# Kernel optimization log

Measured on AMD Instinct MI355X. Metric: run time of the kernel, lower is better.

The kernel has to match this reference:

```python
import jax, jax.numpy as jnp
import numpy as np

B, S, D, E, TOPK = 4, 2048, 1024, 8, 2


def setup_inputs() -> dict:
    key = jax.random.key(0)
    k1, k2, k3 = jax.random.split(key, 3)
    scale = 1.0 / np.sqrt(D)
    return {
        "x": jax.random.normal(k1, (B, S, D), dtype=jnp.float32),
        "gate_w": jax.random.normal(k2, (D, E), dtype=jnp.float32) * scale,
        "gate_b": jnp.zeros((E,), dtype=jnp.float32),
        "expert_w": jax.random.normal(k3, (E, D, D), dtype=jnp.float32) * scale,
        "expert_b": jnp.zeros((E, D), dtype=jnp.float32),
        "top_k": TOPK,
    }


def reference(x, gate_w, gate_b, expert_w, expert_b, top_k):
    # Gating: softmax over experts, then top-k expert indices per token.
    logits = x @ gate_w + gate_b                      # [B, S, E]
    probs = jax.nn.softmax(logits, axis=-1)
    _, top_idx = jax.lax.top_k(probs, top_k)          # [B, S, top_k]
    # Binary membership mask (original multiplies by mask, NOT gate probs).
    mask = jax.nn.one_hot(top_idx, probs.shape[-1], dtype=x.dtype).sum(axis=-2)  # [B, S, E]
    # Dense per-expert linear on all tokens (as in the original loop).
    expert_out = jnp.einsum('bsd,edf->bsef', x, expert_w) + expert_b  # [B, S, E, D]
    # Mask-multiply-accumulate over experts.
    return jnp.einsum('bse,bsef->bsf', mask, expert_out)             # [B, S, D]
```

## Files before the change

### kernel.cpp

```cpp
#include <hip/hip_runtime.h>
#include <stdint.h>

#define T_TOK 8192
#define DD    1024
#define EN    8
#define CPAD  16

#define BM 128
#define BN 128
#define BK 64
#define NT (DD / BK)
#define NWG 4096

#define GATE_NB 512

#define AS1 __attribute__((address_space(1)))
#define AS3 __attribute__((address_space(3)))

typedef __bf16 v8bf __attribute__((ext_vector_type(8)));
typedef float  v4f  __attribute__((ext_vector_type(4)));

__device__ __forceinline__ uint16_t f2b(float f) {
  uint32_t u = __builtin_bit_cast(uint32_t, f);
  u += 0x7FFFu + ((u >> 16) & 1u);
  return (uint16_t)(u >> 16);
}
__device__ __forceinline__ float b2f(uint16_t h) {
  uint32_t u = (uint32_t)h << 16;
  return __builtin_bit_cast(float, u);
}

template <bool WRITE_PIDX>
__global__ __launch_bounds__(256) void prep_kernel(
    const float* __restrict__ x, const float* __restrict__ gw,
    const float* __restrict__ gb, uint16_t* __restrict__ xb,
    int* __restrict__ counts, int* __restrict__ lists, int* __restrict__ pidx,
    const float* __restrict__ w, uint16_t* __restrict__ wt) {
  extern __shared__ __align__(16) uint8_t smem[];
  const int bid = blockIdx.x;
  const int tid = threadIdx.x;

  if (bid >= GATE_NB) {
    float (*tile)[65] = (float(*)[65])smem;
    const int tb = bid - GATE_NB;
    const int e = tb >> 8;
    const int rem = tb & 255;
    const int f0 = (rem & 15) * 64, d0 = (rem >> 4) * 64;
    const float* wsrc = w + ((size_t)e << 20);
    uint16_t* wdst = wt + ((size_t)e << 20);
    const int r4 = tid >> 4;
    const int c4 = (tid & 15) * 4;
#pragma unroll
    for (int i = 0; i < 4; ++i) {
      int row = i * 16 + r4;
      const float4 v = *(const float4*)(wsrc + (size_t)(d0 + row) * DD + f0 + c4);
      tile[row][c4 + 0] = v.x; tile[row][c4 + 1] = v.y;
      tile[row][c4 + 2] = v.z; tile[row][c4 + 3] = v.w;
    }
    __syncthreads();
#pragma unroll
    for (int i = 0; i < 4; ++i) {
      int f = i * 16 + r4;
      ushort4 h;
      h.x = f2b(tile[c4 + 0][f]); h.y = f2b(tile[c4 + 1][f]);
      h.z = f2b(tile[c4 + 2][f]); h.w = f2b(tile[c4 + 3][f]);
      *(ushort4*)(wdst + (size_t)(f0 + f) * DD + d0 + c4) = h;
    }
    return;
  }

  float* sgwt = (float*)smem;
  float (*sx)[DD] = (float(*)[DD])(smem + 32768);
  int* se1 = (int*)(smem + 49152);
  int* se2 = (int*)(smem + 49152 + 64);

#pragma unroll
  for (int i = 0; i < 8; ++i) {
    const int j4 = i * 256 + tid;
    const float4 v = ((const float4*)gw)[j4];
    const int d = j4 >> 1;
    const int e0 = (j4 & 1) * 4;
    sgwt[(e0 + 0) * DD + d] = v.x;
    sgwt[(e0 + 1) * DD + d] = v.y;
    sgwt[(e0 + 2) * DD + d] = v.z;
    sgwt[(e0 + 3) * DD + d] = v.w;
  }
  __syncthreads();

  const int t0 = bid * 16;
  const int wid = tid >> 6, lane = tid & 63;

  for (int r = 0; r < 4; ++r) {
    const int tt = t0 + wid * 4 + r;
    const float4* xg = (const float4*)(x + (size_t)tt * DD);
    float4* sxv = (float4*)sx[wid];
    ushort4* xbv = (ushort4*)(xb + (size_t)tt * DD);
#pragma unroll
    for (int i = 0; i < 4; ++i) {
      float4 v = xg[i * 64 + lane];
      sxv[i * 64 + lane] = v;
      ushort4 h;
      h.x = f2b(v.x); h.y = f2b(v.y); h.z = f2b(v.z); h.w = f2b(v.w);
      xbv[i * 64 + lane] = h;
    }
    asm volatile("s_waitcnt lgkmcnt(0)" ::: "memory");

    double part[8];
#pragma unroll
    for (int e = 0; e < 8; ++e) part[e] = 0.0;
#pragma unroll
    for (int c = 0; c < 16; ++c) {
      const double xd = (double)sx[wid][c * 64 + lane];
#pragma unroll
      for (int e = 0; e < 8; ++e)
        part[e] += xd * (double)sgwt[e * DD + c * 64 + lane];
    }
#pragma unroll
    for (int off = 1; off < 64; off <<= 1) {
#pragma unroll
      for (int e = 0; e < 8; ++e) part[e] += __shfl_xor(part[e], off);
    }
    if (lane == 0) {
      double lg[8];
#pragma unroll
      for (int i = 0; i < 8; ++i) lg[i] = part[i] + (double)gb[i];
      int e1 = 0; double m1 = lg[0];
#pragma unroll
      for (int i = 1; i < 8; ++i) if (lg[i] > m1) { m1 = lg[i]; e1 = i; }
      int e2 = 0; double m2 = -1.0e300;
#pragma unroll
      for (int i = 0; i < 8; ++i) if (i != e1 && lg[i] > m2) { m2 = lg[i]; e2 = i; }
      se1[wid * 4 + r] = e1;
      se2[wid * 4 + r] = e2;
    }
  }
  __syncthreads();

  if (tid < EN) {
    int cnt = 0;
#pragma unroll
    for (int i = 0; i < 16; ++i) cnt += (se1[i] == tid) + (se2[i] == tid);
    int base = atomicAdd(&counts[tid * CPAD], cnt);
    int* dst = lists + tid * T_TOK;
    for (int i = 0; i < 16; ++i) {
      if (se1[i] == tid) {
        if (WRITE_PIDX) pidx[2 * (t0 + i)] = tid * T_TOK + base;
        dst[base++] = t0 + i;
      }
      if (se2[i] == tid) {
        if (WRITE_PIDX) pidx[2 * (t0 + i) + 1] = tid * T_TOK + base;
        dst[base++] = t0 + i;
      }
    }
  }
}

template <bool ATOMIC>
__global__ __launch_bounds__(256, 4) void expert_gemm_kernel(
    const uint16_t* __restrict__ xb, const uint16_t* __restrict__ wt,
    const float* __restrict__ eb, const int* __restrict__ counts,
    const int* __restrict__ lists, uint16_t* __restrict__ dst,
    float* __restrict__ dstf) {
  const int orig = blockIdx.x;
  const int e = orig & 7;
  const int rem = orig >> 3;
  const int m0 = (rem >> 3) * BM;
  const int n0 = (rem & 7) * BN;
  const int cnt = counts[e * CPAD];
  if (m0 >= cnt) return;
  int rows = cnt - m0; if (rows > BM) rows = BM;
  int offsE = 0;
  if (!ATOMIC) {
#pragma unroll
    for (int i = 0; i < EN; ++i) offsE += (i < e) ? counts[i * CPAD] : 0;
  }

  __shared__ uint16_t sA[BM * BK];
  __shared__ uint16_t sB[BN * BK];
  __shared__ int toks[BM];

  const int tid = threadIdx.x;
  if (tid < BM) {
    int rr = tid < rows ? tid : 0;
    toks[tid] = lists[e * T_TOK + m0 + rr];
  }
  __syncthreads();

  const int lane = tid & 63;
  const int wid = tid >> 6;
  const int wm = wid >> 1;
  const int wn = wid & 1;

  v4f acc[4][4];
#pragma unroll
  for (int i = 0; i < 4; ++i)
#pragma unroll
    for (int j = 0; j < 4; ++j) acc[i][j] = (v4f){0.f, 0.f, 0.f, 0.f};

  const int koff = (((tid & 7) ^ ((tid >> 3) & 7)) << 3);
  const uint16_t* wte = wt + ((size_t)e << 20) + (size_t)n0 * DD;
  const uint16_t* aptr[4];
  const uint16_t* bptr[4];
#pragma unroll
  for (int i = 0; i < 4; ++i) {
    int row = i * 32 + (tid >> 3);
    aptr[i] = xb + (size_t)toks[row] * DD + koff;
    bptr[i] = wte + (size_t)row * DD + koff;
  }

  const int c0 = lane >> 4;
  const int rsel = lane & 15;
  const int rx = lane & 7;

  for (int kt = 0; kt < NT; ++kt) {
    const int k0 = kt * BK;
#pragma unroll
    for (int i = 0; i < 4; ++i) {
      int idx = i * 256 + tid;
      __builtin_amdgcn_global_load_lds(
          (const AS1 uint32_t*)(aptr[i] + k0),
          (AS3 uint32_t*)(sA + idx * 8), 16, 0, 0);
      __builtin_amdgcn_global_load_lds(
          (const AS1 uint32_t*)(bptr[i] + k0),
          (AS3 uint32_t*)(sB + idx * 8), 16, 0, 0);
    }
    __syncthreads();

#pragma unroll
    for (int kk = 0; kk < 2; ++kk) {
      v8bf af[4], bfr[4];
#pragma unroll
      for (int m = 0; m < 4; ++m) {
        int row_a = wm * 64 + m * 16 + rsel;
        af[m] = *(const v8bf*)(sA + row_a * BK + (((kk * 4 + c0) ^ rx) << 3));
      }
#pragma unroll
      for (int n = 0; n < 4; ++n) {
        int row_b = wn * 64 + n * 16 + rsel;
        bfr[n] = *(const v8bf*)(sB + row_b * BK + (((kk * 4 + c0) ^ rx) << 3));
      }
#pragma unroll
      for (int m = 0; m < 4; ++m)
#pragma unroll
        for (int n = 0; n < 4; ++n)
          acc[m][n] = __builtin_amdgcn_mfma_f32_16x16x32_bf16(
              af[m], bfr[n], acc[m][n], 0, 0, 0);
    }
    __syncthreads();
  }

  const int col = lane & 15, rq = lane >> 4;
  if (!ATOMIC) {
    uint16_t* base = dst + (size_t)(offsE + m0) * DD + n0 + wn * 64 + col;
#pragma unroll
    for (int m = 0; m < 4; ++m) {
#pragma unroll
      for (int j = 0; j < 4; ++j) {
        int trow = wm * 64 + m * 16 + rq * 4 + j;
        if (trow < rows) {
          uint16_t* orow = base + (size_t)trow * DD;
#pragma unroll
          for (int n = 0; n < 4; ++n) orow[n * 16] = f2b(acc[m][n][j]);
        }
      }
    }
  } else {
    float biasv[4];
#pragma unroll
    for (int n = 0; n < 4; ++n)
      biasv[n] = eb[e * DD + n0 + wn * 64 + n * 16 + col];
#pragma unroll
    for (int m = 0; m < 4; ++m) {
#pragma unroll
      for (int j = 0; j < 4; ++j) {
        int trow = wm * 64 + m * 16 + rq * 4 + j;
        if (trow < rows) {
          float* orow = dstf + (size_t)toks[trow] * DD + n0;
#pragma unroll
          for (int n = 0; n < 4; ++n)
            atomicAdd(orow + wn * 64 + n * 16 + col, acc[m][n][j] + biasv[n]);
        }
      }
    }
  }
}

__global__ __launch_bounds__(256) void combine_kernel(
    const uint16_t* __restrict__ wsO, const int* __restrict__ pidx,
    const int* __restrict__ counts, const float* __restrict__ eb,
    float* __restrict__ out) {
  __shared__ int soff[EN];
  const int tid = threadIdx.x;
  if (tid == 0) {
    int o = 0;
#pragma unroll
    for (int i = 0; i < EN; ++i) { soff[i] = o; o += counts[i * CPAD]; }
  }
  __syncthreads();
  const int t0 = blockIdx.x * 4;
#pragma unroll
  for (int r = 0; r < 4; ++r) {
    const int t = t0 + r;
    const int pi1 = pidx[2 * t], pi2 = pidx[2 * t + 1];
    const int e1 = pi1 >> 13, p1 = pi1 & (T_TOK - 1);
    const int e2 = pi2 >> 13, p2 = pi2 & (T_TOK - 1);
    ushort4 r1 = ((const ushort4*)(wsO + (size_t)(soff[e1] + p1) * DD))[tid];
    ushort4 r2 = ((const ushort4*)(wsO + (size_t)(soff[e2] + p2) * DD))[tid];
    v4f b1 = ((const v4f*)(eb + e1 * DD))[tid];
    v4f b2 = ((const v4f*)(eb + e2 * DD))[tid];
    v4f o;
    o[0] = b2f(r1.x) + b2f(r2.x) + b1[0] + b2[0];
    o[1] = b2f(r1.y) + b2f(r2.y) + b1[1] + b2[1];
    o[2] = b2f(r1.z) + b2f(r2.z) + b1[2] + b2[2];
    o[3] = b2f(r1.w) + b2f(r2.w) + b1[3] + b2[3];
    ((v4f*)(out + (size_t)t * DD))[tid] = o;
  }
}

extern "C" void kernel_launch(void* const* d_in, const int* in_sizes, int n_in,
                              void* d_out, int out_size, void* d_ws, size_t ws_size,
                              hipStream_t stream) {
  const float* x  = (const float*)d_in[0];
  const float* gw = (const float*)d_in[1];
  const float* gb = (const float*)d_in[2];
  const float* ew = (const float*)d_in[3];
  const float* ebias = (const float*)d_in[4];
  float* out = (float*)d_out;

  uint8_t* ws = (uint8_t*)d_ws;
  int* counts = (int*)ws;
  int* lists  = (int*)(ws + 512);
  int* pidx   = (int*)(ws + 512 + 262144);
  uint16_t* xb = (uint16_t*)(ws + 512 + 262144 + 65536);
  uint16_t* wt = (uint16_t*)(ws + 512 + 262144 + 65536 + 16777216);
  uint16_t* wsO = (uint16_t*)(ws + 512 + 262144 + 65536 + 2 * 16777216);
  const size_t need = 512ull + 262144 + 65536 + 2 * 16777216 +
                      (size_t)2 * T_TOK * DD * sizeof(uint16_t);
  const bool use_ws = ws_size >= need;

  hipMemsetAsync(counts, 0, 512, stream);
  if (use_ws) {
    prep_kernel<true><<<GATE_NB + 2048, 256, 49408, stream>>>(
        x, gw, gb, xb, counts, lists, pidx, ew, wt);
    expert_gemm_kernel<false><<<NWG, 256, 0, stream>>>(
        xb, wt, ebias, counts, lists, wsO, nullptr);
    combine_kernel<<<T_TOK / 4, 256, 0, stream>>>(wsO, pidx, counts, ebias, out);
  } else {
    hipMemsetAsync(d_out, 0, (size_t)out_size * sizeof(float), stream);
    prep_kernel<false><<<GATE_NB + 2048, 256, 49408, stream>>>(
        x, gw, gb, xb, counts, lists, pidx, ew, wt);
    expert_gemm_kernel<true><<<NWG, 256, 0, stream>>>(
        xb, wt, ebias, counts, lists, nullptr, out);
  }
}
```

Before: 92.93 us.

## Double-buffer LDS tiles in expert GEMM to overlap global loads with MFMA

```diff
diff --git a/kernel.cpp b/kernel.cpp
--- a/kernel.cpp
+++ b/kernel.cpp
@@ -156,7 +156,7 @@
 }
 
 template <bool ATOMIC>
-__global__ __launch_bounds__(256, 4) void expert_gemm_kernel(
+__global__ __launch_bounds__(256, 2) void expert_gemm_kernel(
     const uint16_t* __restrict__ xb, const uint16_t* __restrict__ wt,
     const float* __restrict__ eb, const int* __restrict__ counts,
     const int* __restrict__ lists, uint16_t* __restrict__ dst,
@@ -175,8 +175,8 @@
     for (int i = 0; i < EN; ++i) offsE += (i < e) ? counts[i * CPAD] : 0;
   }
 
-  __shared__ uint16_t sA[BM * BK];
-  __shared__ uint16_t sB[BN * BK];
+  __shared__ uint16_t sA[2 * BM * BK];
+  __shared__ uint16_t sB[2 * BN * BK];
   __shared__ int toks[BM];
 
   const int tid = threadIdx.x;
@@ -208,36 +208,53 @@
     bptr[i] = wte + (size_t)row * DD + koff;
   }
 
+#define STAGE(buf, k0)                                                          \
+  {                                                                             \
+    _Pragma("unroll")                                                           \
+    for (int i = 0; i < 4; ++i) {                                               \
+      int idx = i * 256 + tid;                                                  \
+      __builtin_amdgcn_global_load_lds(                                         \
+          (const AS1 uint32_t*)(aptr[i] + (k0)),                                \
+          (AS3 uint32_t*)(sA + (buf) * (BM * BK) + idx * 8), 16, 0, 0);         \
+      __builtin_amdgcn_global_load_lds(                                         \
+          (const AS1 uint32_t*)(bptr[i] + (k0)),                                \
+          (AS3 uint32_t*)(sB + (buf) * (BN * BK) + idx * 8), 16, 0, 0);         \
+    }                                                                           \
+  }
+
   const int c0 = lane >> 4;
   const int rsel = lane & 15;
   const int rx = lane & 7;
 
+  STAGE(0, 0);
+  int cur = 0;
   for (int kt = 0; kt < NT; ++kt) {
-    const int k0 = kt * BK;
-#pragma unroll
-    for (int i = 0; i < 4; ++i) {
-      int idx = i * 256 + tid;
-      __builtin_amdgcn_global_load_lds(
-          (const AS1 uint32_t*)(aptr[i] + k0),
-          (AS3 uint32_t*)(sA + idx * 8), 16, 0, 0);
-      __builtin_amdgcn_global_load_lds(
-          (const AS1 uint32_t*)(bptr[i] + k0),
-          (AS3 uint32_t*)(sB + idx * 8), 16, 0, 0);
-    }
-    __syncthreads();
-
+    if (kt + 1 < NT) {
+      STAGE(cur ^ 1, (kt + 1) * BK);
+      __builtin_amdgcn_sched_barrier(0);
+      asm volatile("s_waitcnt vmcnt(8)" ::: "memory");
+    } else {
+      __builtin_amdgcn_sched_barrier(0);
+      asm volatile("s_waitcnt vmcnt(0)" ::: "memory");
+    }
+    __builtin_amdgcn_sched_barrier(0);
+    __builtin_amdgcn_s_barrier();
+    __builtin_amdgcn_sched_barrier(0);
+
+    const uint16_t* a_base = sA + cur * (BM * BK);
+    const uint16_t* b_base = sB + cur * (BN * BK);
 #pragma unroll
     for (int kk = 0; kk < 2; ++kk) {
       v8bf af[4], bfr[4];
 #pragma unroll
       for (int m = 0; m < 4; ++m) {
         int row_a = wm * 64 + m * 16 + rsel;
-        af[m] = *(const v8bf*)(sA + row_a * BK + (((kk * 4 + c0) ^ rx) << 3));
+        af[m] = *(const v8bf*)(a_base + row_a * BK + (((kk * 4 + c0) ^ rx) << 3));
       }
 #pragma unroll
       for (int n = 0; n < 4; ++n) {
         int row_b = wn * 64 + n * 16 + rsel;
-        bfr[n] = *(const v8bf*)(sB + row_b * BK + (((kk * 4 + c0) ^ rx) << 3));
+        bfr[n] = *(const v8bf*)(b_base + row_b * BK + (((kk * 4 + c0) ^ rx) << 3));
       }
 #pragma unroll
       for (int m = 0; m < 4; ++m)
@@ -246,8 +263,11 @@
           acc[m][n] = __builtin_amdgcn_mfma_f32_16x16x32_bf16(
               af[m], bfr[n], acc[m][n], 0, 0, 0);
     }
-    __syncthreads();
-  }
+    __builtin_amdgcn_sched_barrier(0);
+    __builtin_amdgcn_s_barrier();
+    cur ^= 1;
+  }
+#undef STAGE
 
   const int col = lane & 15, rq = lane >> 4;
   if (!ATOMIC) {
```

Measured after the change: 104.2 us. +12.1%, slower.
